# Optimization experiments

Measured on AMD Instinct MI355X. Metric: run time of the kernel, lower is better.

## Reference

```python
import jax, jax.numpy as jnp
import numpy as np

N, E, B, L = 65536, 262144, 512, 1000
IN_DIM, HID, VOCAB = 74, 128, 25
CHANNELS = [HID, 96, 128, IN_DIM, HID]  # protein conv1d filter chain


def _conv1d(x, k):
    # x: [B, C_in, L], k: [C_out, C_in, 3], stride 1, padding 1 (like nn.Conv1d)
    return jax.lax.conv_general_dilated(x, k, (1,), ((1, 1),),
                                        dimension_numbers=('NCH', 'OIH', 'NCH'))


def setup_inputs() -> dict:
    key = jax.random.key(0)
    ks = jax.random.split(key, 20)

    def gl(k, shape, fan_in):
        return jax.random.normal(k, shape, jnp.float32) / np.float32(np.sqrt(fan_in))

    inp = {}
    inp['node_feats'] = jax.random.normal(ks[0], (N, IN_DIM), jnp.float32)
    # GraphConv (conv1): weight [in, hid]
    inp['W_gc'] = gl(ks[1], (IN_DIM, HID), IN_DIM)
    inp['b_gc'] = jnp.zeros((HID,), jnp.float32)
    # MLPNodeReadout: two linears (no activation between, per dgllife default)
    inp['W_ro_in'] = gl(ks[2], (HID, HID), HID)
    inp['b_ro_in'] = jnp.zeros((HID,), jnp.float32)
    inp['W_ro_out'] = gl(ks[3], (HID, HID), HID)
    inp['b_ro_out'] = jnp.zeros((HID,), jnp.float32)
    inp['Wc1'] = gl(ks[4], (HID, HID), HID); inp['bc1'] = jnp.zeros((HID,), jnp.float32)
    inp['Wc2'] = gl(ks[5], (HID, HID), HID); inp['bc2'] = jnp.zeros((HID,), jnp.float32)
    # protein embedding + 4 conv1d layers
    inp['embed'] = jax.random.normal(ks[6], (VOCAB, HID), jnp.float32)
    for i in range(4):
        cin, cout = CHANNELS[i], CHANNELS[i + 1]
        inp['K%d' % (i + 1)] = gl(ks[7 + i], (cout, cin, 3), cin * 3)
        inp['cb%d' % (i + 1)] = jnp.zeros((cout,), jnp.float32)
    # CPI head: Linear(2h,2h)+ReLU, Linear(2h,1)+Sigmoid
    inp['Wf1'] = gl(ks[11], (2 * HID, 2 * HID), 2 * HID); inp['bf1'] = jnp.zeros((2 * HID,), jnp.float32)
    inp['Wf2'] = gl(ks[12], (2 * HID, 1), 2 * HID); inp['bf2'] = jnp.zeros((1,), jnp.float32)
    # graph structure / protein tokens
    inp['edge_src'] = jax.random.randint(ks[13], (E,), 0, N, jnp.int32)
    inp['edge_dst'] = jax.random.randint(ks[14], (E,), 0, N, jnp.int32)
    inp['graph_ids'] = jnp.sort(jax.random.randint(ks[15], (N,), 0, B, jnp.int32))
    inp['protein_seq'] = jax.random.randint(ks[16], (B, L), 0, VOCAB, jnp.int32)
    return inp


def reference(node_feats, W_gc, b_gc, W_ro_in, b_ro_in, W_ro_out, b_ro_out,
              Wc1, bc1, Wc2, bc2, embed, K1, cb1, K2, cb2, K3, cb3, K4, cb4,
              Wf1, bf1, Wf2, bf2, edge_src, edge_dst, graph_ids, protein_seq):
    n = node_feats.shape[0]
    nb = protein_seq.shape[0]
    # dgl.add_self_loop: append self edges
    loop = jnp.arange(n, dtype=edge_src.dtype)
    src = jnp.concatenate([edge_src, loop])
    dst = jnp.concatenate([edge_dst, loop])
    ones = jnp.ones(src.shape[0], jnp.float32)
    deg_out = jax.ops.segment_sum(ones, src, n)  # out-degree (src norm)
    deg_in = jax.ops.segment_sum(ones, dst, n)   # in-degree (dst norm)
    h = node_feats * jax.lax.rsqrt(deg_out)[:, None]
    h = jax.ops.segment_sum(h[src], dst, n) * jax.lax.rsqrt(deg_in)[:, None]
    h = jax.nn.relu(h @ W_gc + b_gc)
    # MLPNodeReadout (sum over nodes per graph), then outer ReLU
    x = (h @ W_ro_in + b_ro_in) @ W_ro_out + b_ro_out
    hg = jax.nn.relu(jax.ops.segment_sum(x, graph_ids, nb))  # [B, HID]
    # compound FC layers (dropout = identity)
    cv = jax.nn.relu(hg @ Wc1 + bc1)
    cv = jax.nn.relu(cv @ Wc2 + bc2)
    pv = jnp.transpose(embed[protein_seq], (0, 2, 1))
    for K, b in ((K1, cb1), (K2, cb2), (K3, cb3), (K4, cb4)):
        pv = jax.nn.relu(_conv1d(pv, K) + b[None, :, None])
    pmax = jnp.max(pv, axis=-1)  # adaptive_max_pool1d(output_size=1) + squeeze
    # CPI head
    z = jnp.concatenate([cv, pmax], axis=1)  # [B, 2*HID]
    z = jax.nn.relu(z @ Wf1 + bf1)
    return jax.nn.sigmoid(z @ Wf2 + bf2)  # [B, 1]
```

## Files before the change

kernel.cpp:

```cpp
#include <hip/hip_runtime.h>
#include <math.h>

#define IN_DIM 74
#define HID 128
#define LSEQ 1000
#define RSA 272
#define RSB 208
#define TILE 48
#define R0 56
#define R1 54
#define R2 52
#define R3 50
#define LDS_BIAS 16384
#define LDS_ACT  18176
#define ACTA_SZ  15232
#define ACTB_SZ  11232
#define LDS_TOTAL 71104

typedef unsigned int u32;
typedef unsigned short u16;

typedef __attribute__((ext_vector_type(8))) short bf16x8;
typedef __attribute__((ext_vector_type(4))) float f32x4;

__device__ __forceinline__ u16 f2bf(float f){
  u32 u = __float_as_uint(f);
  u32 r = (u + 0x7fffu + ((u >> 16) & 1u)) >> 16;
  return (u16)r;
}
__device__ __forceinline__ u32 pack2(float x, float y){
  return (u32)f2bf(x) | ((u32)f2bf(y) << 16);
}

__global__ void k_deg_init(int* out_cnt, int* in_cnt, int N){
  int i = blockIdx.x*256 + threadIdx.x;
  if (i < N){ out_cnt[i] = 0; in_cnt[i] = 0; }
}
__global__ void k_cnt_edge(const int* __restrict__ src, const int* __restrict__ dst,
                           int* out_cnt, int* in_cnt, int E){
  int e = blockIdx.x*256 + threadIdx.x;
  if (e < E){ atomicAdd(&out_cnt[src[e]], 1); atomicAdd(&in_cnt[dst[e]], 1); }
}
__global__ void k_scan1(const int* __restrict__ cnt, int* pref, int* bsum, int N){
  __shared__ int buf[256];
  int t = threadIdx.x, i = blockIdx.x*256 + t;
  int v = (i < N) ? cnt[i] : 0;
  buf[t] = v; __syncthreads();
  for (int o = 1; o < 256; o <<= 1){
    int tv = (t >= o) ? buf[t-o] : 0;
    __syncthreads(); buf[t] += tv; __syncthreads();
  }
  if (i < N) pref[i] = buf[t] - v;
  if (t == 255) bsum[blockIdx.x] = buf[255];
}
__global__ void k_scan2(int* bsum, int nb){
  __shared__ int buf[1024];
  int t = threadIdx.x;
  int v = (t < nb) ? bsum[t] : 0;
  buf[t] = v; __syncthreads();
  for (int o = 1; o < 1024; o <<= 1){
    int tv = (t >= o) ? buf[t-o] : 0;
    __syncthreads(); buf[t] += tv; __syncthreads();
  }
  if (t < nb) bsum[t] = buf[t] - v;
}
__global__ void k_scan3(const int* __restrict__ pref, const int* __restrict__ bsum,
                        int* offs, int* cur, int N){
  int i = blockIdx.x*256 + threadIdx.x;
  if (i < N){ int o = pref[i] + bsum[blockIdx.x]; offs[i] = o; cur[i] = o; }
}
__global__ void k_csr_fill(const int* __restrict__ src, const int* __restrict__ dst,
                           int* cur, int* csr_src, int E){
  int e = blockIdx.x*256 + threadIdx.x;
  if (e < E){ int slot = atomicAdd(&cur[dst[e]], 1); csr_src[slot] = src[e]; }
}
__global__ __launch_bounds__(256) void k_gather(const float* __restrict__ nf,
    const int* __restrict__ csr_src, const int* __restrict__ offs,
    const int* __restrict__ in_cnt, const int* __restrict__ out_cnt,
    float* __restrict__ h_agg, int N){
  int wid = threadIdx.x >> 6, lane = threadIdx.x & 63;
  int d = blockIdx.x*4 + wid;
  if (d >= N) return;
  int beg = offs[d], num = in_cnt[d];
  const float* row = nf + (size_t)d*IN_DIM;
  float ws = rsqrtf((float)out_cnt[d] + 1.f);
  float a0 = row[lane]*ws, a1 = 0.f;
  if (lane < IN_DIM-64) a1 = row[64+lane]*ws;
  for (int j = 0; j < num; ++j){
    int s = csr_src[beg + j];
    float w = rsqrtf((float)out_cnt[s] + 1.f);
    const float* rs = nf + (size_t)s*IN_DIM;
    a0 += rs[lane]*w;
    if (lane < IN_DIM-64) a1 += rs[64+lane]*w;
  }
  float sc = rsqrtf((float)num + 1.f);
  float* hp = h_agg + (size_t)d*IN_DIM;
  hp[lane] = a0*sc;
  if (lane < IN_DIM-64) hp[64+lane] = a1*sc;
}
__global__ __launch_bounds__(256) void k_gc_gemm(const float* __restrict__ h_agg,
        const float* __restrict__ W, const float* __restrict__ bias,
        float* __restrict__ h, int N){
  __shared__ float Wl[IN_DIM*HID];
  __shared__ float rowsT[IN_DIM][36];
  int base = blockIdx.x * 32;
  for (int idx = threadIdx.x; idx < IN_DIM*HID; idx += 256) Wl[idx] = W[idx];
  for (int idx = threadIdx.x; idx < 32*IN_DIM; idx += 256){
    int r = idx / IN_DIM, k = idx - r*IN_DIM;
    rowsT[k][r] = (base + r < N) ? h_agg[(size_t)(base+r)*IN_DIM + k] : 0.f;
  }
  __syncthreads();
  int c = threadIdx.x & 127, rh = threadIdx.x >> 7;
  float acc[16];
  #pragma unroll
  for (int i = 0; i < 16; ++i) acc[i] = 0.f;
  for (int k = 0; k < IN_DIM; ++k){
    float w = Wl[k*HID + c];
    const float4* rp = (const float4*)&rowsT[k][rh*16];
    float4 r0 = rp[0], r1 = rp[1], r2 = rp[2], r3 = rp[3];
    acc[0] += r0.x*w; acc[1] += r0.y*w; acc[2] += r0.z*w; acc[3] += r0.w*w;
    acc[4] += r1.x*w; acc[5] += r1.y*w; acc[6] += r1.z*w; acc[7] += r1.w*w;
    acc[8] += r2.x*w; acc[9] += r2.y*w; acc[10] += r2.z*w; acc[11] += r2.w*w;
    acc[12] += r3.x*w; acc[13] += r3.y*w; acc[14] += r3.z*w; acc[15] += r3.w*w;
  }
  float bv = bias[c];
  #pragma unroll
  for (int i = 0; i < 16; ++i){
    int r = base + rh*16 + i;
    if (r < N) h[(size_t)r*HID + c] = fmaxf(acc[i] + bv, 0.f);
  }
}
__global__ __launch_bounds__(128) void k_graph_tail(const float* __restrict__ h,
    const int* __restrict__ gid,
    const float* __restrict__ W_ri, const float* __restrict__ b_ri,
    const float* __restrict__ W_ro, const float* __restrict__ b_ro,
    const float* __restrict__ Wc1, const float* __restrict__ bc1,
    const float* __restrict__ Wc2, const float* __restrict__ bc2,
    float* __restrict__ z, int N){
  __shared__ float va[128], vb[128];
  __shared__ int bounds[2];
  int g = blockIdx.x, c = threadIdx.x;
  if (c < 2){
    int target = g + c, lo = 0, hi = N;
    while (lo < hi){ int mid = (lo+hi)>>1; if (gid[mid] < target) lo = mid+1; else hi = mid; }
    bounds[c] = lo;
  }
  __syncthreads();
  int lo = bounds[0], hi = bounds[1];
  float s = 0.f;
  for (int i = lo; i < hi; ++i) s += h[(size_t)i*HID + c];
  va[c] = s;
  float cn = (float)(hi - lo);
  __syncthreads();
  s = 0.f;
  for (int k = 0; k < 128; ++k) s += va[k]*W_ri[k*128 + c];
  vb[c] = s + b_ri[c]*cn;
  __syncthreads();
  s = 0.f;
  for (int k = 0; k < 128; ++k) s += vb[k]*W_ro[k*128 + c];
  va[c] = fmaxf(s + b_ro[c]*cn, 0.f);
  __syncthreads();
  s = 0.f;
  for (int k = 0; k < 128; ++k) s += va[k]*Wc1[k*128 + c];
  vb[c] = fmaxf(s + bc1[c], 0.f);
  __syncthreads();
  s = 0.f;
  for (int k = 0; k < 128; ++k) s += vb[k]*Wc2[k*128 + c];
  z[(size_t)g*256 + c] = fmaxf(s + bc2[c], 0.f);
}

__global__ void k_zero_zp(float* z, int total){
  int i = blockIdx.x*256 + threadIdx.x;
  if (i < total){ int b = i >> 7, c = i & 127; z[(size_t)b*256 + 128 + c] = 0.f; }
}
__global__ void k_prepack2(const float* __restrict__ Kw, u16* __restrict__ A2p,
                           int CIN, int CPAD, int COUT, int KS){
  int idx = blockIdx.x*256 + threadIdx.x;
  if (idx >= KS*4096) return;
  int ks = idx >> 12, rem = idx & 4095;
  int co = rem >> 5, kk = rem & 31;
  int k = ks*32 + kk;
  int t = k / CPAD, ci = k - t*CPAD;
  float v = (co < COUT && ci < CIN) ? Kw[((size_t)co*CIN + ci)*3 + t] : 0.f;
  A2p[idx] = f2bf(v);
}
__global__ void k_biaspack(const float* b1, const float* b2, const float* b3,
                           const float* b4, float* outb){
  int i = threadIdx.x;
  float v = 0.f;
  if (i < 96) v = b1[i];
  else if (i < 224) v = b2[i-96];
  else if (i < 320){ int c = i-224; v = (c < 74) ? b3[c] : 0.f; }
  else if (i < 448) v = b4[i-320];
  if (i < 448) outb[i] = v;
}

__device__ __forceinline__ void stage8k(char* lds, int tid, const u16* src, int pbuf){
  const char* s = (const char*)src;
  char* d = lds + pbuf*8192;
  __builtin_amdgcn_global_load_lds(
    (const __attribute__((address_space(1))) unsigned*)(s + tid*16),
    (__attribute__((address_space(3))) unsigned*)(d + tid*16), 16, 0, 0);
  __builtin_amdgcn_global_load_lds(
    (const __attribute__((address_space(1))) unsigned*)(s + 4096 + tid*16),
    (__attribute__((address_space(3))) unsigned*)(d + 4096 + tid*16), 16, 0, 0);
}

template<int KS, int M, int TPC, int RS_IN, int RCAP>
__device__ __forceinline__ void conv_phases(char* lds, const char* actIn,
    const u16* apk, const u16* nextA, int p0, int co0, int lm, int cg, int tid,
    f32x4 (&acc)[M][4])
{
  #pragma unroll
  for (int m = 0; m < M; ++m)
    #pragma unroll
    for (int n = 0; n < 4; ++n) acc[m][n] = (f32x4){0.f,0.f,0.f,0.f};
  #pragma unroll
  for (int ks = 0; ks < KS; ++ks){
    const u16* nsrc = (ks+1 < KS) ? apk + (size_t)(ks+1)*4096 : nextA;
    if (nsrc){
      stage8k(lds, tid, nsrc, (p0+ks+1)&1);
      asm volatile("s_waitcnt vmcnt(2)");
    } else {
      asm volatile("s_waitcnt vmcnt(0)");
    }
    __builtin_amdgcn_s_barrier();
    __builtin_amdgcn_sched_barrier(0);
    const char* wb = lds + ((p0+ks)&1)*8192;
    bf16x8 Af[M];
    #pragma unroll
    for (int m = 0; m < M; ++m)
      Af[m] = *(const bf16x8*)(wb + (co0 + m*16 + lm)*64 + cg*16);
    const int tap = ks / TPC;
    const int c16 = (ks - tap*TPC)*4 + cg;
    bf16x8 Bf[4];
    #pragma unroll
    for (int n = 0; n < 4; ++n){
      int raw = n*16 + lm + tap;
      int row = raw < RCAP ? raw : RCAP;
      Bf[n] = *(const bf16x8*)(actIn + row*RS_IN + c16*16);
    }
    __builtin_amdgcn_s_setprio(1);
    #pragma unroll
    for (int m = 0; m < M; ++m)
      #pragma unroll
      for (int n = 0; n < 4; ++n)
        acc[m][n] = __builtin_amdgcn_mfma_f32_16x16x32_bf16(Af[m], Bf[n], acc[m][n], 0, 0, 0);
    __builtin_amdgcn_s_setprio(0);
    asm volatile("s_waitcnt lgkmcnt(0)");
    __builtin_amdgcn_s_barrier();
  }
}

template<int M>
__device__ __forceinline__ void epi_store(char* actOut, int RS_OUT,
    const float* lbias, int boff, int co0, int lm, int cg,
    int lbase, int nrows, f32x4 (&acc)[M][4])
{
  #pragma unroll
  for (int m = 0; m < M; ++m){
    int co = co0 + m*16 + cg*4;
    float4 bb = *(const float4*)(lbias + boff + co);
    #pragma unroll
    for (int n = 0; n < 4; ++n){
      int r1 = n*16 + lm;
      if (r1 < nrows){
        int l = lbase + r1;
        u32 lo = 0, hi = 0;
        if ((unsigned)l < (unsigned)LSEQ){
          f32x4 a = acc[m][n];
          lo = pack2(fmaxf(a[0]+bb.x, 0.f), fmaxf(a[1]+bb.y, 0.f));
          hi = pack2(fmaxf(a[2]+bb.z, 0.f), fmaxf(a[3]+bb.w, 0.f));
        }
        uint2 st; st.x = lo; st.y = hi;
        *(uint2*)(actOut + r1*RS_OUT + co*2) = st;
      }
    }
  }
  asm volatile("s_waitcnt lgkmcnt(0)");
}

__device__ __forceinline__ void epi_pool(const float* lbias, int boff,
    int co0, int lm, int cg, int l0, float* __restrict__ z, int b, f32x4 (&acc)[4][4])
{
  float mxv[4][4];
  #pragma unroll
  for (int m = 0; m < 4; ++m)
    #pragma unroll
    for (int j = 0; j < 4; ++j) mxv[m][j] = 0.f;
  #pragma unroll
  for (int m = 0; m < 4; ++m){
    float4 bb = *(const float4*)(lbias + boff + co0 + m*16 + cg*4);
    const float* bv = (const float*)&bb;
    #pragma unroll
    for (int n = 0; n < 4; ++n){
      int r1 = n*16 + lm;
      int l = l0 + r1;
      if (r1 < TILE && l < LSEQ){
        #pragma unroll
        for (int j = 0; j < 4; ++j)
          mxv[m][j] = fmaxf(mxv[m][j], fmaxf(acc[m][n][j] + bv[j], 0.f));
      }
    }
  }
  #pragma unroll
  for (int o = 1; o <= 8; o <<= 1)
    #pragma unroll
    for (int m = 0; m < 4; ++m)
      #pragma unroll
      for (int j = 0; j < 4; ++j)
        mxv[m][j] = fmaxf(mxv[m][j], __shfl_xor(mxv[m][j], o));
  if (lm == 0){
    float* zrow = z + (size_t)b*256 + 128;
    #pragma unroll
    for (int m = 0; m < 4; ++m)
      #pragma unroll
      for (int j = 0; j < 4; ++j)
        atomicMax((u32*)(zrow + co0 + m*16 + cg*4 + j), __float_as_uint(mxv[m][j]));
  }
}

__global__ __launch_bounds__(256, 2) void k_protein(
    const int* __restrict__ seq, const float* __restrict__ emb,
    const u16* __restrict__ A1, const u16* __restrict__ A2,
    const u16* __restrict__ A3, const u16* __restrict__ A4,
    const float* __restrict__ ball, float* __restrict__ z)
{
  __shared__ __align__(16) char lds[LDS_TOTAL];
  const int tid = threadIdx.x;
  const int lane = tid & 63, wid = tid >> 6;
  const int lm = lane & 15, cg = lane >> 4;
  const int tl = wid >> 1;
  const int h  = wid & 1;
  const int b  = blockIdx.y;
  const int l0 = (blockIdx.x*2 + tl) * TILE;

  for (int i = tid; i < 448; i += 256) ((float*)(lds + LDS_BIAS))[i] = ball[i];

  for (int idx = tid; idx < 2*R0*16; idx += 256){
    int t2 = idx / (R0*16), rem = idx - t2*(R0*16);
    int r = rem >> 4, p = rem & 15;
    int ll0 = (blockIdx.x*2 + t2) * TILE;
    int l = ll0 - 4 + r;
    uint4 st = make_uint4(0u,0u,0u,0u);
    if ((unsigned)l < (unsigned)LSEQ){
      int tok = seq[b*LSEQ + l];
      const float4* e = (const float4*)(emb + (size_t)tok*HID + p*8);
      float4 v0 = e[0], v1 = e[1];
      st.x = pack2(v0.x, v0.y); st.y = pack2(v0.z, v0.w);
      st.z = pack2(v1.x, v1.y); st.w = pack2(v1.z, v1.w);
    }
    *(uint4*)(lds + LDS_ACT + t2*ACTA_SZ + r*RSA + p*16) = st;
  }
  asm volatile("s_waitcnt vmcnt(0)");
  stage8k(lds, tid, A1, 0);
  asm volatile("s_waitcnt lgkmcnt(0)");
  __builtin_amdgcn_s_barrier();

  char* actA = lds + LDS_ACT + tl*ACTA_SZ;
  char* actB = lds + LDS_ACT + 2*ACTA_SZ + tl*ACTB_SZ;
  const float* lbias = (const float*)(lds + LDS_BIAS);

  {
    f32x4 acc[3][4];
    conv_phases<12,3,4,RSA,R0-1>(lds, actA, A1, A2, 0, h*48, lm, cg, tid, acc);
    epi_store<3>(actB, RSB, lbias, 0, h*48, lm, cg, l0-3, R1, acc);
  }
  {
    f32x4 acc[4][4];
    conv_phases<9,4,3,RSB,R1-1>(lds, actB, A2, A3, 12, h*64, lm, cg, tid, acc);
    epi_store<4>(actA, RSA, lbias, 96, h*64, lm, cg, l0-2, R2, acc);
  }
  {
    f32x4 acc[3][4];
    conv_phases<12,3,4,RSA,R2-1>(lds, actA, A3, A4, 21, h*48, lm, cg, tid, acc);
    epi_store<3>(actB, RSB, lbias, 224, h*48, lm, cg, l0-1, R3, acc);
  }
  {
    f32x4 acc[4][4];
    conv_phases<9,4,3,RSB,R3-1>(lds, actB, A4, nullptr, 33, h*64, lm, cg, tid, acc);
    epi_pool(lbias, 320, h*64, lm, cg, l0, z, b, acc);
  }
}

__global__ __launch_bounds__(256) void k_fc_head(const float* __restrict__ z,
    const float* __restrict__ Wf1, const float* __restrict__ bf1,
    const float* __restrict__ Wf2, const float* __restrict__ bf2v,
    float* __restrict__ out){
  __shared__ float za[256];
  __shared__ float red[4];
  int r = blockIdx.x, c = threadIdx.x;
  za[c] = z[(size_t)r*256 + c];
  __syncthreads();
  float s = 0.f;
  for (int k = 0; k < 256; ++k) s += za[k]*Wf1[(size_t)k*256 + c];
  s = fmaxf(s + bf1[c], 0.f);
  float p = s * Wf2[c];
  for (int o = 32; o; o >>= 1) p += __shfl_xor(p, o);
  if ((c & 63) == 0) red[c >> 6] = p;
  __syncthreads();
  if (c == 0) out[r] = 1.f/(1.f + __expf(-(red[0]+red[1]+red[2]+red[3] + bf2v[0])));
}

extern "C" void kernel_launch(void* const* d_in, const int* in_sizes, int n_in,
                              void* d_out, int out_size, void* d_ws, size_t ws_size,
                              hipStream_t stream){
  const float* nf   = (const float*)d_in[0];
  const float* W_gc = (const float*)d_in[1];
  const float* b_gc = (const float*)d_in[2];
  const float* W_ri = (const float*)d_in[3];
  const float* b_ri = (const float*)d_in[4];
  const float* W_ro = (const float*)d_in[5];
  const float* b_ro = (const float*)d_in[6];
  const float* Wc1  = (const float*)d_in[7];
  const float* bc1  = (const float*)d_in[8];
  const float* Wc2  = (const float*)d_in[9];
  const float* bc2  = (const float*)d_in[10];
  const float* emb  = (const float*)d_in[11];
  const float* K1 = (const float*)d_in[12]; const float* cb1 = (const float*)d_in[13];
  const float* K2 = (const float*)d_in[14]; const float* cb2 = (const float*)d_in[15];
  const float* K3 = (const float*)d_in[16]; const float* cb3 = (const float*)d_in[17];
  const float* K4 = (const float*)d_in[18]; const float* cb4 = (const float*)d_in[19];
  const float* Wf1 = (const float*)d_in[20]; const float* bf1 = (const float*)d_in[21];
  const float* Wf2 = (const float*)d_in[22]; const float* bf2v = (const float*)d_in[23];
  const int* esrc = (const int*)d_in[24];
  const int* edst = (const int*)d_in[25];
  const int* gids = (const int*)d_in[26];
  const int* seq  = (const int*)d_in[27];
  float* out = (float*)d_out;

  int N = in_sizes[26];
  int E = in_sizes[24];
  int B = out_size;
  int nb = (N + 255)/256;

  char* ws = (char*)d_ws;
  size_t off = 0;
  auto take = [&](size_t bytes)->char*{
    char* p = ws + off; off = (off + bytes + 255) & ~(size_t)255; return p;
  };
  float* z      = (float*)take((size_t)B*2*HID*4);
  int* out_cnt  = (int*)take((size_t)N*4);
  int* in_cnt   = (int*)take((size_t)N*4);
  int* pref     = (int*)take((size_t)N*4);
  int* offs     = (int*)take((size_t)N*4);
  int* cur      = (int*)take((size_t)N*4);
  int* bsum     = (int*)take(1024*4);
  int* csr_src  = (int*)take((size_t)E*4);
  u16* A1 = (u16*)take((size_t)12*8192);
  u16* A2 = (u16*)take((size_t)9*8192);
  u16* A3 = (u16*)take((size_t)12*8192);
  u16* A4 = (u16*)take((size_t)9*8192);
  float* ball = (float*)take(448*4);
  float* h_agg = (float*)take((size_t)N*IN_DIM*4);
  float* h     = (float*)take((size_t)N*HID*4);

  k_zero_zp<<<(B*HID + 255)/256, 256, 0, stream>>>(z, B*HID);
  k_prepack2<<<(12*4096+255)/256, 256, 0, stream>>>(K1, A1, 128, 128,  96, 12);
  k_prepack2<<<( 9*4096+255)/256, 256, 0, stream>>>(K2, A2,  96,  96, 128,  9);
  k_prepack2<<<(12*4096+255)/256, 256, 0, stream>>>(K3, A3,  74, 128,  74, 12);
  k_prepack2<<<( 9*4096+255)/256, 256, 0, stream>>>(K4, A4,  74,  96, 128,  9);
  k_biaspack<<<1, 512, 0, stream>>>(cb1, cb2, cb3, cb4, ball);

  k_deg_init<<<nb, 256, 0, stream>>>(out_cnt, in_cnt, N);
  k_cnt_edge<<<(E+255)/256, 256, 0, stream>>>(esrc, edst, out_cnt, in_cnt, E);
  k_scan1<<<nb, 256, 0, stream>>>(in_cnt, pref, bsum, N);
  k_scan2<<<1, 1024, 0, stream>>>(bsum, nb);
  k_scan3<<<nb, 256, 0, stream>>>(pref, bsum, offs, cur, N);
  k_csr_fill<<<(E+255)/256, 256, 0, stream>>>(esrc, edst, cur, csr_src, E);
  k_gather<<<(N+3)/4, 256, 0, stream>>>(nf, csr_src, offs, in_cnt, out_cnt, h_agg, N);
  k_gc_gemm<<<(N+31)/32, 256, 0, stream>>>(h_agg, W_gc, b_gc, h, N);
  k_graph_tail<<<B, 128, 0, stream>>>(h, gids, W_ri, b_ri, W_ro, b_ro,
                                      Wc1, bc1, Wc2, bc2, z, N);

  dim3 pgrid(11, B);
  k_protein<<<pgrid, 256, 0, stream>>>(seq, emb, A1, A2, A3, A4, ball, z);

  k_fc_head<<<B, 256, 0, stream>>>(z, Wf1, bf1, Wf2, bf2v, out);
}
```

Baseline: 465.6 us.

## Give each wave full output channels over its own tile and swizzle weight LDS

Each of the four waves now owns a separate 48-position sequence tile and computes every output channel for it, rather than two waves splitting the channels of one tile. Each B fragment load now feeds twice as many MFMAs, and each staged weight slice serves four tiles instead of two. The block count per sequence drops from 11 to 6. Weight packing gets an XOR swizzle on the 16-byte groups to cut LDS bank conflicts on A-fragment reads. In exchange the accumulator arrays double, so launch bounds fall to one block per CU and LDS use rises, which lowers occupancy and latency hiding. With 24 tile slots per sequence there is also wasted tail work.

```diff
diff --git a/kernel.cpp b/kernel.cpp
--- a/kernel.cpp
+++ b/kernel.cpp
@@ -15,7 +15,8 @@
 #define LDS_ACT  18176
 #define ACTA_SZ  15232
 #define ACTB_SZ  11232
-#define LDS_TOTAL 71104
+#define ACTB_BASE (LDS_ACT + 4*ACTA_SZ)
+#define LDS_TOTAL (ACTB_BASE + 4*ACTB_SZ)
 
 typedef unsigned int u32;
 typedef unsigned short u16;
@@ -182,7 +183,8 @@
   int k = ks*32 + kk;
   int t = k / CPAD, ci = k - t*CPAD;
   float v = (co < COUT && ci < CIN) ? Kw[((size_t)co*CIN + ci)*3 + t] : 0.f;
-  A2p[idx] = f2bf(v);
+  int sl2 = (kk >> 3) ^ ((co >> 1) & 3);
+  A2p[(size_t)ks*4096 + co*32 + sl2*8 + (kk & 7)] = f2bf(v);
 }
 __global__ void k_biaspack(const float* b1, const float* b2, const float* b3,
                            const float* b4, float* outb){
@@ -208,7 +210,7 @@
 
 template<int KS, int M, int TPC, int RS_IN, int RCAP>
 __device__ __forceinline__ void conv_phases(char* lds, const char* actIn,
-    const u16* apk, const u16* nextA, int p0, int co0, int lm, int cg, int tid,
+    const u16* apk, const u16* nextA, int p0, int lm, int cg, int scg, int tid,
     f32x4 (&acc)[M][4])
 {
   #pragma unroll
@@ -230,7 +232,7 @@
     bf16x8 Af[M];
     #pragma unroll
     for (int m = 0; m < M; ++m)
-      Af[m] = *(const bf16x8*)(wb + (co0 + m*16 + lm)*64 + cg*16);
+      Af[m] = *(const bf16x8*)(wb + (m*16 + lm)*64 + scg*16);
     const int tap = ks / TPC;
     const int c16 = (ks - tap*TPC)*4 + cg;
     bf16x8 Bf[4];
@@ -254,12 +256,12 @@
 
 template<int M>
 __device__ __forceinline__ void epi_store(char* actOut, int RS_OUT,
-    const float* lbias, int boff, int co0, int lm, int cg,
+    const float* lbias, int boff, int lm, int cg,
     int lbase, int nrows, f32x4 (&acc)[M][4])
 {
   #pragma unroll
   for (int m = 0; m < M; ++m){
-    int co = co0 + m*16 + cg*4;
+    int co = m*16 + cg*4;
     float4 bb = *(const float4*)(lbias + boff + co);
     #pragma unroll
     for (int n = 0; n < 4; ++n){
@@ -281,16 +283,16 @@
 }
 
 __device__ __forceinline__ void epi_pool(const float* lbias, int boff,
-    int co0, int lm, int cg, int l0, float* __restrict__ z, int b, f32x4 (&acc)[4][4])
+    int lm, int cg, int l0, float* __restrict__ z, int b, f32x4 (&acc)[8][4])
 {
-  float mxv[4][4];
-  #pragma unroll
-  for (int m = 0; m < 4; ++m)
+  float mxv[8][4];
+  #pragma unroll
+  for (int m = 0; m < 8; ++m)
     #pragma unroll
     for (int j = 0; j < 4; ++j) mxv[m][j] = 0.f;
   #pragma unroll
-  for (int m = 0; m < 4; ++m){
-    float4 bb = *(const float4*)(lbias + boff + co0 + m*16 + cg*4);
+  for (int m = 0; m < 8; ++m){
+    float4 bb = *(const float4*)(lbias + boff + m*16 + cg*4);
     const float* bv = (const float*)&bb;
     #pragma unroll
     for (int n = 0; n < 4; ++n){
@@ -306,21 +308,21 @@
   #pragma unroll
   for (int o = 1; o <= 8; o <<= 1)
     #pragma unroll
-    for (int m = 0; m < 4; ++m)
+    for (int m = 0; m < 8; ++m)
       #pragma unroll
       for (int j = 0; j < 4; ++j)
         mxv[m][j] = fmaxf(mxv[m][j], __shfl_xor(mxv[m][j], o));
   if (lm == 0){
     float* zrow = z + (size_t)b*256 + 128;
     #pragma unroll
-    for (int m = 0; m < 4; ++m)
+    for (int m = 0; m < 8; ++m)
       #pragma unroll
       for (int j = 0; j < 4; ++j)
-        atomicMax((u32*)(zrow + co0 + m*16 + cg*4 + j), __float_as_uint(mxv[m][j]));
-  }
-}
-
-__global__ __launch_bounds__(256, 2) void k_protein(
+        atomicMax((u32*)(zrow + m*16 + cg*4 + j), __float_as_uint(mxv[m][j]));
+  }
+}
+
+__global__ __launch_bounds__(256, 1) void k_protein(
     const int* __restrict__ seq, const float* __restrict__ emb,
     const u16* __restrict__ A1, const u16* __restrict__ A2,
     const u16* __restrict__ A3, const u16* __restrict__ A4,
@@ -330,17 +332,16 @@
   const int tid = threadIdx.x;
   const int lane = tid & 63, wid = tid >> 6;
   const int lm = lane & 15, cg = lane >> 4;
-  const int tl = wid >> 1;
-  const int h  = wid & 1;
+  const int scg = cg ^ ((lm >> 1) & 3);
   const int b  = blockIdx.y;
-  const int l0 = (blockIdx.x*2 + tl) * TILE;
+  const int l0 = (blockIdx.x*4 + wid) * TILE;
 
   for (int i = tid; i < 448; i += 256) ((float*)(lds + LDS_BIAS))[i] = ball[i];
 
-  for (int idx = tid; idx < 2*R0*16; idx += 256){
+  for (int idx = tid; idx < 4*R0*16; idx += 256){
     int t2 = idx / (R0*16), rem = idx - t2*(R0*16);
     int r = rem >> 4, p = rem & 15;
-    int ll0 = (blockIdx.x*2 + t2) * TILE;
+    int ll0 = (blockIdx.x*4 + t2) * TILE;
     int l = ll0 - 4 + r;
     uint4 st = make_uint4(0u,0u,0u,0u);
     if ((unsigned)l < (unsigned)LSEQ){
@@ -357,29 +358,29 @@
   asm volatile("s_waitcnt lgkmcnt(0)");
   __builtin_amdgcn_s_barrier();
 
-  char* actA = lds + LDS_ACT + tl*ACTA_SZ;
-  char* actB = lds + LDS_ACT + 2*ACTA_SZ + tl*ACTB_SZ;
+  char* actA = lds + LDS_ACT + wid*ACTA_SZ;
+  char* actB = lds + ACTB_BASE + wid*ACTB_SZ;
   const float* lbias = (const float*)(lds + LDS_BIAS);
 
   {
-    f32x4 acc[3][4];
-    conv_phases<12,3,4,RSA,R0-1>(lds, actA, A1, A2, 0, h*48, lm, cg, tid, acc);
-    epi_store<3>(actB, RSB, lbias, 0, h*48, lm, cg, l0-3, R1, acc);
+    f32x4 acc[6][4];
+    conv_phases<12,6,4,RSA,R0-1>(lds, actA, A1, A2, 0, lm, cg, scg, tid, acc);
+    epi_store<6>(actB, RSB, lbias, 0, lm, cg, l0-3, R1, acc);
   }
   {
-    f32x4 acc[4][4];
-    conv_phases<9,4,3,RSB,R1-1>(lds, actB, A2, A3, 12, h*64, lm, cg, tid, acc);
-    epi_store<4>(actA, RSA, lbias, 96, h*64, lm, cg, l0-2, R2, acc);
+    f32x4 acc[8][4];
+    conv_phases<9,8,3,RSB,R1-1>(lds, actB, A2, A3, 12, lm, cg, scg, tid, acc);
+    epi_store<8>(actA, RSA, lbias, 96, lm, cg, l0-2, R2, acc);
   }
   {
-    f32x4 acc[3][4];
-    conv_phases<12,3,4,RSA,R2-1>(lds, actA, A3, A4, 21, h*48, lm, cg, tid, acc);
-    epi_store<3>(actB, RSB, lbias, 224, h*48, lm, cg, l0-1, R3, acc);
+    f32x4 acc[6][4];
+    conv_phases<12,6,4,RSA,R2-1>(lds, actA, A3, A4, 21, lm, cg, scg, tid, acc);
+    epi_store<6>(actB, RSB, lbias, 224, lm, cg, l0-1, R3, acc);
   }
   {
-    f32x4 acc[4][4];
-    conv_phases<9,4,3,RSB,R3-1>(lds, actB, A4, nullptr, 33, h*64, lm, cg, tid, acc);
-    epi_pool(lbias, 320, h*64, lm, cg, l0, z, b, acc);
+    f32x4 acc[8][4];
+    conv_phases<9,8,3,RSB,R3-1>(lds, actB, A4, nullptr, 33, lm, cg, scg, tid, acc);
+    epi_pool(lbias, 320, lm, cg, l0, z, b, acc);
   }
 }
 
@@ -473,7 +474,7 @@
   k_graph_tail<<<B, 128, 0, stream>>>(h, gids, W_ri, b_ri, W_ro, b_ro,
                                       Wc1, bc1, Wc2, bc2, z, N);
 
-  dim3 pgrid(11, B);
+  dim3 pgrid(6, B);
   k_protein<<<pgrid, 256, 0, stream>>>(seq, emb, A1, A2, A3, A4, ball, z);
 
   k_fc_head<<<B, 256, 0, stream>>>(z, Wf1, bf1, Wf2, bf2v, out);
```

After: 589.4 us. 26.6% more time.

## Triple-buffer conv weight staging with one barrier, swizzle LDS, fuse setup kernels

Applied to the files above, without the earlier changes.

Merges the zeroing, weight prepack, bias pack and degree-init kernels into one setup launch, which removes several small launches. The conv weight chunks are now stored contiguously and staged into three LDS buffers two chunks ahead, so each K-step needs one barrier instead of two. The weight layout gets an XOR swizzle to cut LDS bank conflicts on the A-fragment reads. The cost is 8KB more LDS per block, which may reduce occupancy, plus the risk of a race with only one barrier per step.

```diff
diff --git a/kernel.cpp b/kernel.cpp
--- a/kernel.cpp
+++ b/kernel.cpp
@@ -11,11 +11,13 @@
 #define R1 54
 #define R2 52
 #define R3 50
-#define LDS_BIAS 16384
-#define LDS_ACT  18176
+#define NCHUNK 42
+#define LDS_BIAS 24576
+#define LDS_ACT  26368
 #define ACTA_SZ  15232
 #define ACTB_SZ  11232
-#define LDS_TOTAL 71104
+#define ACTB_BASE (LDS_ACT + 2*ACTA_SZ)
+#define LDS_TOTAL (ACTB_BASE + 2*ACTB_SZ)
 
 typedef unsigned int u32;
 typedef unsigned short u16;
@@ -32,10 +34,6 @@
   return (u32)f2bf(x) | ((u32)f2bf(y) << 16);
 }
 
-__global__ void k_deg_init(int* out_cnt, int* in_cnt, int N){
-  int i = blockIdx.x*256 + threadIdx.x;
-  if (i < N){ out_cnt[i] = 0; in_cnt[i] = 0; }
-}
 __global__ void k_cnt_edge(const int* __restrict__ src, const int* __restrict__ dst,
                            int* out_cnt, int* in_cnt, int E){
   int e = blockIdx.x*256 + threadIdx.x;
@@ -169,30 +167,45 @@
   z[(size_t)g*256 + c] = fmaxf(s + bc2[c], 0.f);
 }
 
-__global__ void k_zero_zp(float* z, int total){
-  int i = blockIdx.x*256 + threadIdx.x;
-  if (i < total){ int b = i >> 7, c = i & 127; z[(size_t)b*256 + 128 + c] = 0.f; }
-}
-__global__ void k_prepack2(const float* __restrict__ Kw, u16* __restrict__ A2p,
-                           int CIN, int CPAD, int COUT, int KS){
+__global__ void k_setup(const float* __restrict__ K1, const float* __restrict__ K2,
+                        const float* __restrict__ K3, const float* __restrict__ K4,
+                        const float* __restrict__ cb1, const float* __restrict__ cb2,
+                        const float* __restrict__ cb3, const float* __restrict__ cb4,
+                        u16* __restrict__ AW, float* __restrict__ ball,
+                        float* __restrict__ z, int* __restrict__ out_cnt,
+                        int* __restrict__ in_cnt, int N, int B){
   int idx = blockIdx.x*256 + threadIdx.x;
-  if (idx >= KS*4096) return;
-  int ks = idx >> 12, rem = idx & 4095;
-  int co = rem >> 5, kk = rem & 31;
-  int k = ks*32 + kk;
-  int t = k / CPAD, ci = k - t*CPAD;
-  float v = (co < COUT && ci < CIN) ? Kw[((size_t)co*CIN + ci)*3 + t] : 0.f;
-  A2p[idx] = f2bf(v);
-}
-__global__ void k_biaspack(const float* b1, const float* b2, const float* b3,
-                           const float* b4, float* outb){
-  int i = threadIdx.x;
-  float v = 0.f;
-  if (i < 96) v = b1[i];
-  else if (i < 224) v = b2[i-96];
-  else if (i < 320){ int c = i-224; v = (c < 74) ? b3[c] : 0.f; }
-  else if (i < 448) v = b4[i-320];
-  if (i < 448) outb[i] = v;
+  if (idx < NCHUNK*4096){
+    int g = idx >> 12, rem = idx & 4095;
+    int co = rem >> 5, kk = rem & 31;
+    const float* Kw; int CIN, CPAD, COUT, ksl;
+    if (g < 12)      { Kw = K1; CIN = 128; CPAD = 128; COUT =  96; ksl = g; }
+    else if (g < 21) { Kw = K2; CIN =  96; CPAD =  96; COUT = 128; ksl = g-12; }
+    else if (g < 33) { Kw = K3; CIN =  74; CPAD = 128; COUT =  74; ksl = g-21; }
+    else             { Kw = K4; CIN =  74; CPAD =  96; COUT = 128; ksl = g-33; }
+    int k = ksl*32 + kk;
+    int t = k / CPAD, ci = k - t*CPAD;
+    float v = (co < COUT && ci < CIN) ? Kw[((size_t)co*CIN + ci)*3 + t] : 0.f;
+    int sl2 = (kk >> 3) ^ ((co >> 1) & 3);
+    AW[(size_t)g*4096 + co*32 + sl2*8 + (kk & 7)] = f2bf(v);
+    return;
+  }
+  idx -= NCHUNK*4096;
+  if (idx < 448){
+    float v = 0.f;
+    if (idx < 96) v = cb1[idx];
+    else if (idx < 224) v = cb2[idx-96];
+    else if (idx < 320){ int c = idx-224; v = (c < 74) ? cb3[c] : 0.f; }
+    else v = cb4[idx-320];
+    ball[idx] = v;
+    return;
+  }
+  idx -= 448;
+  if (idx < B*128){ z[(size_t)(idx>>7)*256 + 128 + (idx&127)] = 0.f; return; }
+  idx -= B*128;
+  if (idx < 2*N){
+    if (idx < N) out_cnt[idx] = 0; else in_cnt[idx-N] = 0;
+  }
 }
 
 __device__ __forceinline__ void stage8k(char* lds, int tid, const u16* src, int pbuf){
@@ -206,9 +219,9 @@
     (__attribute__((address_space(3))) unsigned*)(d + 4096 + tid*16), 16, 0, 0);
 }
 
-template<int KS, int M, int TPC, int RS_IN, int RCAP>
+template<int KS, int G0, int M, int TPC, int RS_IN, int RCAP>
 __device__ __forceinline__ void conv_phases(char* lds, const char* actIn,
-    const u16* apk, const u16* nextA, int p0, int co0, int lm, int cg, int tid,
+    const u16* __restrict__ AW, int co0, int lm, int cg, int scg, int tid,
     f32x4 (&acc)[M][4])
 {
   #pragma unroll
@@ -217,20 +230,17 @@
     for (int n = 0; n < 4; ++n) acc[m][n] = (f32x4){0.f,0.f,0.f,0.f};
   #pragma unroll
   for (int ks = 0; ks < KS; ++ks){
-    const u16* nsrc = (ks+1 < KS) ? apk + (size_t)(ks+1)*4096 : nextA;
-    if (nsrc){
-      stage8k(lds, tid, nsrc, (p0+ks+1)&1);
-      asm volatile("s_waitcnt vmcnt(2)");
-    } else {
-      asm volatile("s_waitcnt vmcnt(0)");
-    }
+    const int g = G0 + ks;
+    if (g + 1 < NCHUNK) asm volatile("s_waitcnt vmcnt(2)");
+    else                asm volatile("s_waitcnt vmcnt(0)");
     __builtin_amdgcn_s_barrier();
     __builtin_amdgcn_sched_barrier(0);
-    const char* wb = lds + ((p0+ks)&1)*8192;
+    if (g + 2 < NCHUNK) stage8k(lds, tid, AW + (size_t)(g+2)*4096, (g+2)%3);
+    const char* wb = lds + (g%3)*8192;
     bf16x8 Af[M];
     #pragma unroll
     for (int m = 0; m < M; ++m)
-      Af[m] = *(const bf16x8*)(wb + (co0 + m*16 + lm)*64 + cg*16);
+      Af[m] = *(const bf16x8*)(wb + (co0 + m*16 + lm)*64 + scg*16);
     const int tap = ks / TPC;
     const int c16 = (ks - tap*TPC)*4 + cg;
     bf16x8 Bf[4];
@@ -248,7 +258,6 @@
         acc[m][n] = __builtin_amdgcn_mfma_f32_16x16x32_bf16(Af[m], Bf[n], acc[m][n], 0, 0, 0);
     __builtin_amdgcn_s_setprio(0);
     asm volatile("s_waitcnt lgkmcnt(0)");
-    __builtin_amdgcn_s_barrier();
   }
 }
 
@@ -322,14 +331,14 @@
 
 __global__ __launch_bounds__(256, 2) void k_protein(
     const int* __restrict__ seq, const float* __restrict__ emb,
-    const u16* __restrict__ A1, const u16* __restrict__ A2,
-    const u16* __restrict__ A3, const u16* __restrict__ A4,
-    const float* __restrict__ ball, float* __restrict__ z)
+    const u16* __restrict__ AW, const float* __restrict__ ball,
+    float* __restrict__ z)
 {
   __shared__ __align__(16) char lds[LDS_TOTAL];
   const int tid = threadIdx.x;
   const int lane = tid & 63, wid = tid >> 6;
   const int lm = lane & 15, cg = lane >> 4;
+  const int scg = cg ^ ((lm >> 1) & 3);
   const int tl = wid >> 1;
   const int h  = wid & 1;
   const int b  = blockIdx.y;
@@ -353,32 +362,32 @@
     *(uint4*)(lds + LDS_ACT + t2*ACTA_SZ + r*RSA + p*16) = st;
   }
   asm volatile("s_waitcnt vmcnt(0)");
-  stage8k(lds, tid, A1, 0);
+  stage8k(lds, tid, AW, 0);
+  stage8k(lds, tid, AW + 4096, 1);
   asm volatile("s_waitcnt lgkmcnt(0)");
-  __builtin_amdgcn_s_barrier();
 
   char* actA = lds + LDS_ACT + tl*ACTA_SZ;
-  char* actB = lds + LDS_ACT + 2*ACTA_SZ + tl*ACTB_SZ;
+  char* actB = lds + ACTB_BASE + tl*ACTB_SZ;
   const float* lbias = (const float*)(lds + LDS_BIAS);
 
   {
     f32x4 acc[3][4];
-    conv_phases<12,3,4,RSA,R0-1>(lds, actA, A1, A2, 0, h*48, lm, cg, tid, acc);
+    conv_phases<12,0,3,4,RSA,R0-1>(lds, actA, AW, h*48, lm, cg, scg, tid, acc);
     epi_store<3>(actB, RSB, lbias, 0, h*48, lm, cg, l0-3, R1, acc);
   }
   {
     f32x4 acc[4][4];
-    conv_phases<9,4,3,RSB,R1-1>(lds, actB, A2, A3, 12, h*64, lm, cg, tid, acc);
+    conv_phases<9,12,4,3,RSB,R1-1>(lds, actB, AW, h*64, lm, cg, scg, tid, acc);
     epi_store<4>(actA, RSA, lbias, 96, h*64, lm, cg, l0-2, R2, acc);
   }
   {
     f32x4 acc[3][4];
-    conv_phases<12,3,4,RSA,R2-1>(lds, actA, A3, A4, 21, h*48, lm, cg, tid, acc);
+    conv_phases<12,21,3,4,RSA,R2-1>(lds, actA, AW, h*48, lm, cg, scg, tid, acc);
     epi_store<3>(actB, RSB, lbias, 224, h*48, lm, cg, l0-1, R3, acc);
   }
   {
     f32x4 acc[4][4];
-    conv_phases<9,4,3,RSB,R3-1>(lds, actB, A4, nullptr, 33, h*64, lm, cg, tid, acc);
+    conv_phases<9,33,4,3,RSB,R3-1>(lds, actB, AW, h*64, lm, cg, scg, tid, acc);
     epi_pool(lbias, 320, h*64, lm, cg, l0, z, b, acc);
   }
 }
@@ -447,22 +456,15 @@
   int* cur      = (int*)take((size_t)N*4);
   int* bsum     = (int*)take(1024*4);
   int* csr_src  = (int*)take((size_t)E*4);
-  u16* A1 = (u16*)take((size_t)12*8192);
-  u16* A2 = (u16*)take((size_t)9*8192);
-  u16* A3 = (u16*)take((size_t)12*8192);
-  u16* A4 = (u16*)take((size_t)9*8192);
-  float* ball = (float*)take(448*4);
-  float* h_agg = (float*)take((size_t)N*IN_DIM*4);
-  float* h     = (float*)take((size_t)N*HID*4);
-
-  k_zero_zp<<<(B*HID + 255)/256, 256, 0, stream>>>(z, B*HID);
-  k_prepack2<<<(12*4096+255)/256, 256, 0, stream>>>(K1, A1, 128, 128,  96, 12);
-  k_prepack2<<<( 9*4096+255)/256, 256, 0, stream>>>(K2, A2,  96,  96, 128,  9);
-  k_prepack2<<<(12*4096+255)/256, 256, 0, stream>>>(K3, A3,  74, 128,  74, 12);
-  k_prepack2<<<( 9*4096+255)/256, 256, 0, stream>>>(K4, A4,  74,  96, 128,  9);
-  k_biaspack<<<1, 512, 0, stream>>>(cb1, cb2, cb3, cb4, ball);
-
-  k_deg_init<<<nb, 256, 0, stream>>>(out_cnt, in_cnt, N);
+  u16* AW       = (u16*)take((size_t)NCHUNK*8192);
+  float* ball   = (float*)take(448*4);
+  float* h_agg  = (float*)take((size_t)N*IN_DIM*4);
+  float* h      = (float*)take((size_t)N*HID*4);
+
+  int setup_total = NCHUNK*4096 + 448 + B*128 + 2*N;
+  k_setup<<<(setup_total+255)/256, 256, 0, stream>>>(K1, K2, K3, K4, cb1, cb2, cb3, cb4,
+                                                     AW, ball, z, out_cnt, in_cnt, N, B);
+
   k_cnt_edge<<<(E+255)/256, 256, 0, stream>>>(esrc, edst, out_cnt, in_cnt, E);
   k_scan1<<<nb, 256, 0, stream>>>(in_cnt, pref, bsum, N);
   k_scan2<<<1, 1024, 0, stream>>>(bsum, nb);
@@ -474,7 +476,7 @@
                                       Wc1, bc1, Wc2, bc2, z, N);
 
   dim3 pgrid(11, B);
-  k_protein<<<pgrid, 256, 0, stream>>>(seq, emb, A1, A2, A3, A4, ball, z);
+  k_protein<<<pgrid, 256, 0, stream>>>(seq, emb, AW, ball, z);
 
   k_fc_head<<<B, 256, 0, stream>>>(z, Wf1, bf1, Wf2, bf2v, out);
 }
```

Result: faster. 435.7 us (-6.4%).
